# Kernel tuning notes

Hardware: AMD Instinct MI355X
Metric: run time of the kernel (lower is better)

## Reference

```python
import jax, jax.numpy as jnp
import numpy as np

N_NODES = 50000
N_EDGES = 800000
IN_FEATS = 128
OUT_FEATS = 64


def setup_inputs() -> dict:
    key = jax.random.key(0)
    k1, k2, k3, k4, k5, k6 = jax.random.split(key, 6)
    feat = jax.random.normal(k1, (N_NODES, IN_FEATS), dtype=jnp.float32)
    edge_src = jax.random.randint(k2, (N_EDGES,), 0, N_NODES, dtype=jnp.int64)
    edge_dst = jax.random.randint(k3, (N_EDGES,), 0, N_NODES, dtype=jnp.int64)
    eweight = jax.random.uniform(k4, (N_EDGES,), dtype=jnp.float32)
    W = jax.random.normal(k5, (OUT_FEATS, IN_FEATS), dtype=jnp.float32) * (1.0 / np.sqrt(IN_FEATS))
    b = jax.random.normal(k6, (OUT_FEATS,), dtype=jnp.float32) * 0.01
    return {"feat": feat, "edge_src": edge_src, "edge_dst": edge_dst,
            "eweight": eweight, "W": W, "b": b}


def reference(feat, edge_src, edge_dst, eweight, W, b):
    # Linear: [N, in] @ [in, out] + [out]
    h = jnp.einsum('ni,oi->no', feat, W) + b
    # u_mul_e: gather src features, scale by per-edge weight -> [E, out]
    m = h[edge_src] * eweight[:, None]
    # sum reduce over dst -> [N, out]
    out = jax.ops.segment_sum(m, edge_dst, num_segments=N_NODES)
    return out
```

## Files before the change

kernel.cpp:

```cpp
#include <hip/hip_runtime.h>

#define IN_FEATS 128
#define OUT_FEATS 64
#define TM 64
#define ALD 136
#define BW_LOG 6
#define BWIDTH 64
#define MAX_NB 1024
#define SE_PER_BLK 8192
#define MAX_BUCKET 3072

typedef short bf16x8 __attribute__((ext_vector_type(8)));
typedef float f32x4 __attribute__((ext_vector_type(4)));

__device__ inline unsigned short f2bf(float f) {
    unsigned u = __float_as_uint(f);
    u += 0x7FFFu + ((u >> 16) & 1u);
    return (unsigned short)(u >> 16);
}
__device__ inline float bf2f_lo(unsigned v) { return __uint_as_float(v << 16); }
__device__ inline float bf2f_hi(unsigned v) { return __uint_as_float(v & 0xFFFF0000u); }
__device__ inline ushort4 cvt4(float4 t) {
    ushort4 s; s.x = f2bf(t.x); s.y = f2bf(t.y); s.z = f2bf(t.z); s.w = f2bf(t.w);
    return s;
}

__global__ __launch_bounds__(256) void coarse_hist(
    const int* __restrict__ edst, int* __restrict__ ghist, int n_edges, int nb)
{
    __shared__ int hist[MAX_NB];
    const int tid = threadIdx.x;
    for (int i = tid; i < nb; i += 256) hist[i] = 0;
    __syncthreads();

    const int n4 = n_edges >> 2;
    const int4* ed4 = (const int4*)edst;
    for (int i = blockIdx.x * 256 + tid; i < n4; i += gridDim.x * 256) {
        int4 d = ed4[i];
        atomicAdd(&hist[d.x >> BW_LOG], 1);
        atomicAdd(&hist[d.y >> BW_LOG], 1);
        atomicAdd(&hist[d.z >> BW_LOG], 1);
        atomicAdd(&hist[d.w >> BW_LOG], 1);
    }
    if (blockIdx.x == 0 && tid < (n_edges & 3))
        atomicAdd(&hist[edst[n4 * 4 + tid] >> BW_LOG], 1);
    __syncthreads();
    for (int i = tid; i < nb; i += 256)
        if (hist[i]) atomicAdd(&ghist[i], hist[i]);
}

__global__ __launch_bounds__(256) void coarse_scan(
    const int* __restrict__ ghist, int* __restrict__ goff,
    int* __restrict__ gcur, int nb)
{
    __shared__ int wsum[4];
    __shared__ int wpre[4];
    const int tid  = threadIdx.x;
    const int lane = tid & 63;
    const int wv   = tid >> 6;
    int i0 = tid * 4;
    int v[4];
    int s = 0;
#pragma unroll
    for (int j = 0; j < 4; ++j) v[j] = (i0 + j < nb) ? ghist[i0 + j] : 0;
#pragma unroll
    for (int j = 0; j < 4; ++j) { int t = v[j]; v[j] = s; s += t; }
    int inc = s;
    for (int off = 1; off < 64; off <<= 1) {
        int t = __shfl_up(inc, off, 64);
        if (lane >= off) inc += t;
    }
    int wexcl = inc - s;
    if (lane == 63) wsum[wv] = inc;
    __syncthreads();
    if (tid == 0) {
        int a = 0;
        for (int k = 0; k < 4; ++k) { wpre[k] = a; a += wsum[k]; }
    }
    __syncthreads();
    int tbase = wpre[wv] + wexcl;
#pragma unroll
    for (int j = 0; j < 4; ++j) {
        int idx = i0 + j;
        if (idx < nb) { int e = tbase + v[j]; goff[idx] = e; gcur[idx] = e; }
    }
    if (tid == 0) goff[nb] = wpre[3] + wsum[3];
}

__global__ __launch_bounds__(256) void stage_linear(
    const float* __restrict__ feat, const float* __restrict__ W,
    const float* __restrict__ b, unsigned short* __restrict__ h,
    const int* __restrict__ esrc, const int* __restrict__ edst,
    const float* __restrict__ ew, int* __restrict__ gcur,
    int2* __restrict__ gstage, int n_nodes, int n_edges, int nb, int nstage)
{
    __shared__ union {
        struct { unsigned short As[TM * ALD]; unsigned short Ws[OUT_FEATS * ALD]; } lin;
        struct { int cntA[MAX_NB]; int cntB[MAX_NB]; int base[MAX_NB]; } st;
    } sm;
    const int tid = threadIdx.x;

    if ((int)blockIdx.x < nstage) {
        int* cntA = sm.st.cntA;
        int* cntB = sm.st.cntB;
        int* base = sm.st.base;
        const int e0 = blockIdx.x * SE_PER_BLK;
        const int e1 = min(e0 + SE_PER_BLK, n_edges);

        for (int i = tid; i < nb; i += 256) { cntA[i] = 0; cntB[i] = 0; }
        __syncthreads();
        for (int e = e0 + tid; e < e1; e += 256)
            atomicAdd(&cntA[edst[e] >> BW_LOG], 1);
        __syncthreads();
        for (int i = tid; i < nb; i += 256) {
            int c = cntA[i];
            base[i] = c ? atomicAdd(&gcur[i], c) : 0;
        }
        __syncthreads();
        for (int e = e0 + tid; e < e1; e += 256) {
            int d  = edst[e];
            int bb = d >> BW_LOG;
            int rk = atomicAdd(&cntB[bb], 1);
            gstage[base[bb] + rk] =
                make_int2(((d & (BWIDTH - 1)) << 16) | esrc[e],
                          __float_as_int(ew[e]));
        }
    } else {
        unsigned short* As = sm.lin.As;
        unsigned short* Ws = sm.lin.Ws;
        const int row0 = ((int)blockIdx.x - nstage) * TM;

        {
            const int c  = tid & 63;
            const int kb = (tid >> 6) * 32;
            const float4* wrow = (const float4*)(W + (size_t)c * IN_FEATS + kb);
#pragma unroll
            for (int i = 0; i < 8; ++i)
                *((ushort4*)&Ws[c * ALD + kb + i * 4]) = cvt4(wrow[i]);
        }
        {
#pragma unroll
            for (int i = 0; i < 8; ++i) {
                int flat = i * 256 + tid;
                int r  = flat >> 5;
                int kc = flat & 31;
                int gr = row0 + r;
                float4 t = (gr < n_nodes)
                    ? ((const float4*)(feat + (size_t)gr * IN_FEATS))[kc]
                    : make_float4(0.f, 0.f, 0.f, 0.f);
                *((ushort4*)&As[r * ALD + kc * 4]) = cvt4(t);
            }
        }
        __syncthreads();

        const int w    = tid >> 6;
        const int lane = tid & 63;
        const int m    = lane & 15;
        const int quad = lane >> 4;
        const int koff = quad * 8;

        f32x4 acc[4];
#pragma unroll
        for (int t = 0; t < 4; ++t) acc[t] = (f32x4){0.f, 0.f, 0.f, 0.f};

#pragma unroll
        for (int chunk = 0; chunk < 4; ++chunk) {
            const int kc = chunk * 32 + koff;
            bf16x8 a = *((const bf16x8*)&As[(w * 16 + m) * ALD + kc]);
#pragma unroll
            for (int t = 0; t < 4; ++t) {
                bf16x8 bfr = *((const bf16x8*)&Ws[(t * 16 + m) * ALD + kc]);
                acc[t] = __builtin_amdgcn_mfma_f32_16x16x32_bf16(a, bfr, acc[t], 0, 0, 0);
            }
        }

#pragma unroll
        for (int t = 0; t < 4; ++t) {
            const int col = t * 16 + m;
            const float bias = b[col];
#pragma unroll
            for (int i = 0; i < 4; ++i) {
                int r = row0 + w * 16 + quad * 4 + i;
                if (r < n_nodes)
                    h[(size_t)r * OUT_FEATS + col] = f2bf(acc[t][i] + bias);
            }
        }
    }
}

__global__ __launch_bounds__(256) void bin_sort(
    int2* __restrict__ gstage, const int* __restrict__ goff,
    int2* __restrict__ seg, int n_nodes, int nb)
{
    __shared__ int2 recs[MAX_BUCKET];
    __shared__ int cnt[BWIDTH];
    __shared__ int cur[BWIDTH];
    const int tid = threadIdx.x;
    const int b   = blockIdx.x;
    const int s0  = goff[b], s1 = goff[b + 1];
    const int m   = s1 - s0;

    if (tid < BWIDTH) cnt[tid] = 0;
    __syncthreads();

    for (int i = tid; i < m; i += 256) {
        int2 r = gstage[s0 + i];
        recs[i] = r;
        atomicAdd(&cnt[(r.x >> 16) & 63], 1);
    }
    __syncthreads();

    if (tid < 64) {
        int v = cnt[tid];
        int inc = v;
        for (int o = 1; o < 64; o <<= 1) {
            int t = __shfl_up(inc, o, 64);
            if (tid >= o) inc += t;
        }
        int excl = inc - v;
        cur[tid] = excl;
        int node = b * BWIDTH + tid;
        if (node < n_nodes) seg[node] = make_int2(s0 + excl, s0 + excl + v);
    }
    __syncthreads();

    for (int i = tid; i < m; i += 256) {
        int2 r = recs[i];
        int pos = atomicAdd(&cur[(r.x >> 16) & 63], 1);
        gstage[s0 + pos] = r;
    }
}

__global__ __launch_bounds__(256) void gather_kernel(
    const unsigned short* __restrict__ h, const int2* __restrict__ seg,
    const int2* __restrict__ perm2, float* __restrict__ out, int n_nodes)
{
    const int wid  = (blockIdx.x * blockDim.x + threadIdx.x) >> 6;
    const int lane = threadIdx.x & 63;
    const int g    = lane >> 5;
    const int f2   = lane & 31;
    const int node = wid * 2 + g;
    const unsigned* h32 = (const unsigned*)h;

    int2 se = (node < n_nodes) ? seg[node] : make_int2(0, 0);
    const int len = se.y - se.x;
    const int olen = __shfl_xor(len, 32, 64);
    const int omax = max(len, olen);

    float a0 = 0.f, a1 = 0.f;
    for (int u = 0; u < omax; u += 8) {
        int2 r[8]; unsigned hv[8];
#pragma unroll
        for (int k = 0; k < 8; ++k) {
            int uk  = u + k;
            int pos = (uk < len) ? (se.x + uk) : (len > 0 ? se.y - 1 : 0);
            r[k] = perm2[pos];
        }
#pragma unroll
        for (int k = 0; k < 8; ++k)
            hv[k] = h32[(size_t)(r[k].x & 0xFFFF) * 32 + f2];
#pragma unroll
        for (int k = 0; k < 8; ++k) {
            float w = (u + k < len) ? __int_as_float(r[k].y) : 0.f;
            a0 += w * bf2f_lo(hv[k]);
            a1 += w * bf2f_hi(hv[k]);
        }
    }
    if (node < n_nodes) {
        float2 o; o.x = a0; o.y = a1;
        *((float2*)&out[(size_t)node * OUT_FEATS + 2 * f2]) = o;
    }
}

__global__ __launch_bounds__(256) void scatter_kernel(
    const unsigned short* __restrict__ h, const int* __restrict__ esrc,
    const int* __restrict__ edst, const float* __restrict__ ew,
    float* __restrict__ out, int n_edges)
{
    const int lane = threadIdx.x & 63;
    const int wave = threadIdx.x >> 6;
    const int stride = gridDim.x * 4;
    for (int e = blockIdx.x * 4 + wave; e < n_edges; e += stride) {
        const int s = esrc[e];
        const int d = edst[e];
        const float w = ew[e];
        atomicAdd(out + (size_t)d * OUT_FEATS + lane,
                  bf2f_lo((unsigned)h[(size_t)s * OUT_FEATS + lane]) * w);
    }
}

extern "C" void kernel_launch(void* const* d_in, const int* in_sizes, int n_in,
                              void* d_out, int out_size, void* d_ws, size_t ws_size,
                              hipStream_t stream) {
    const float* feat = (const float*)d_in[0];
    const int*   esrc = (const int*)d_in[1];
    const int*   edst = (const int*)d_in[2];
    const float* ew   = (const float*)d_in[3];
    const float* W    = (const float*)d_in[4];
    const float* b    = (const float*)d_in[5];
    float* out = (float*)d_out;

    const int n_nodes = in_sizes[0] / IN_FEATS;
    const int n_edges = in_sizes[1];
    const int nb = (n_nodes + BWIDTH - 1) >> BW_LOG;
    const int nlin = (n_nodes + TM - 1) / TM;
    const int nstage = (n_edges + SE_PER_BLK - 1) / SE_PER_BLK;

    char* wsb = (char*)d_ws;
    unsigned short* h = (unsigned short*)wsb;
    size_t off_ghist = (((size_t)n_nodes * OUT_FEATS * sizeof(unsigned short)) + 15) & ~(size_t)15;
    size_t sz_ghist  = (((size_t)nb * sizeof(int)) + 15) & ~(size_t)15;
    size_t off_goff  = off_ghist + sz_ghist;
    size_t sz_goff   = (((size_t)(nb + 1) * sizeof(int)) + 15) & ~(size_t)15;
    size_t off_gcur  = off_goff + sz_goff;
    size_t sz_gcur   = (((size_t)nb * sizeof(int)) + 15) & ~(size_t)15;
    size_t off_seg   = off_gcur + sz_gcur;
    size_t sz_seg    = (((size_t)n_nodes * sizeof(int2)) + 15) & ~(size_t)15;
    size_t off_stage = off_seg + sz_seg;
    size_t needed    = off_stage + (size_t)n_edges * sizeof(int2);

    bool binnable = (nb <= MAX_NB) && (n_nodes < 65536) &&
                    ((size_t)n_edges / (size_t)nb * 2 + 256 <= MAX_BUCKET);

    if (ws_size >= needed && binnable) {
        int*  ghist  = (int*)(wsb + off_ghist);
        int*  goff   = (int*)(wsb + off_goff);
        int*  gcur   = (int*)(wsb + off_gcur);
        int2* seg    = (int2*)(wsb + off_seg);
        int2* gstage = (int2*)(wsb + off_stage);
        hipMemsetAsync(ghist, 0, (size_t)nb * sizeof(int), stream);
        coarse_hist<<<128, 256, 0, stream>>>(edst, ghist, n_edges, nb);
        coarse_scan<<<1, 256, 0, stream>>>(ghist, goff, gcur, nb);
        stage_linear<<<nstage + nlin, 256, 0, stream>>>(
            feat, W, b, h, esrc, edst, ew, gcur, gstage,
            n_nodes, n_edges, nb, nstage);
        bin_sort<<<nb, 256, 0, stream>>>(gstage, goff, seg, n_nodes, nb);
        const int gwaves = (n_nodes + 1) / 2;
        gather_kernel<<<(gwaves + 3) / 4, 256, 0, stream>>>(
            h, seg, gstage, out, n_nodes);
    } else {
        stage_linear<<<nlin, 256, 0, stream>>>(
            feat, W, b, h, esrc, edst, ew, nullptr, nullptr,
            n_nodes, n_edges, nb, 0);
        hipMemsetAsync(d_out, 0, (size_t)out_size * sizeof(float), stream);
        scatter_kernel<<<8192, 256, 0, stream>>>(h, esrc, edst, ew, out, n_edges);
    }
}
```

Before: 154.6 us.

## Register-cache staged edges and reuse first-pass atomic ranks for scatter

Each staging thread now loads 8 consecutive edges with vectorized int4/float4 loads, keeps them in registers, and records the rank returned by its single LDS atomicAdd pass. The second counting pass and its re-read of edge arrays are removed, and the scatter writes directly with the saved ranks. The per-block edge count drops to 2048, so there are four times as many staging blocks, each with fewer nb-sized init and global-atomic loops amortized over less work. Global atomics on gcur rise with the larger block count, and scatter order within a bucket changes.

```diff
diff --git a/kernel.cpp b/kernel.cpp
--- a/kernel.cpp
+++ b/kernel.cpp
@@ -7,7 +7,7 @@
 #define BW_LOG 6
 #define BWIDTH 64
 #define MAX_NB 1024
-#define SE_PER_BLK 8192
+#define SE_PER_BLK 2048
 #define MAX_BUCKET 3072
 
 typedef short bf16x8 __attribute__((ext_vector_type(8)));
@@ -96,34 +96,53 @@
 {
     __shared__ union {
         struct { unsigned short As[TM * ALD]; unsigned short Ws[OUT_FEATS * ALD]; } lin;
-        struct { int cntA[MAX_NB]; int cntB[MAX_NB]; int base[MAX_NB]; } st;
+        struct { int cnt[MAX_NB]; int base[MAX_NB]; } st;
     } sm;
     const int tid = threadIdx.x;
 
     if ((int)blockIdx.x < nstage) {
-        int* cntA = sm.st.cntA;
-        int* cntB = sm.st.cntB;
+        int* cnt  = sm.st.cnt;
         int* base = sm.st.base;
-        const int e0 = blockIdx.x * SE_PER_BLK;
-        const int e1 = min(e0 + SE_PER_BLK, n_edges);
-
-        for (int i = tid; i < nb; i += 256) { cntA[i] = 0; cntB[i] = 0; }
+        for (int i = tid; i < nb; i += 256) cnt[i] = 0;
         __syncthreads();
-        for (int e = e0 + tid; e < e1; e += 256)
-            atomicAdd(&cntA[edst[e] >> BW_LOG], 1);
+
+        const int e0 = blockIdx.x * SE_PER_BLK + tid * 8;
+        int dk[8]; int sk[8]; float wk[8]; int bk[8]; int rk[8];
+        if (e0 + 7 < n_edges) {
+            *((int4*)&dk[0]) = *((const int4*)&edst[e0]);
+            *((int4*)&dk[4]) = *((const int4*)&edst[e0 + 4]);
+            *((int4*)&sk[0]) = *((const int4*)&esrc[e0]);
+            *((int4*)&sk[4]) = *((const int4*)&esrc[e0 + 4]);
+            *((float4*)&wk[0]) = *((const float4*)&ew[e0]);
+            *((float4*)&wk[4]) = *((const float4*)&ew[e0 + 4]);
+#pragma unroll
+            for (int i = 0; i < 8; ++i) {
+                bk[i] = dk[i] >> BW_LOG;
+                rk[i] = atomicAdd(&cnt[bk[i]], 1);
+            }
+        } else {
+#pragma unroll
+            for (int i = 0; i < 8; ++i) {
+                int e = e0 + i;
+                if (e < n_edges) {
+                    dk[i] = edst[e]; sk[i] = esrc[e]; wk[i] = ew[e];
+                    bk[i] = dk[i] >> BW_LOG;
+                    rk[i] = atomicAdd(&cnt[bk[i]], 1);
+                } else bk[i] = -1;
+            }
+        }
         __syncthreads();
         for (int i = tid; i < nb; i += 256) {
-            int c = cntA[i];
+            int c = cnt[i];
             base[i] = c ? atomicAdd(&gcur[i], c) : 0;
         }
         __syncthreads();
-        for (int e = e0 + tid; e < e1; e += 256) {
-            int d  = edst[e];
-            int bb = d >> BW_LOG;
-            int rk = atomicAdd(&cntB[bb], 1);
-            gstage[base[bb] + rk] =
-                make_int2(((d & (BWIDTH - 1)) << 16) | esrc[e],
-                          __float_as_int(ew[e]));
+#pragma unroll
+        for (int i = 0; i < 8; ++i) {
+            if (bk[i] >= 0)
+                gstage[base[bk[i]] + rk[i]] =
+                    make_int2(((dk[i] & (BWIDTH - 1)) << 16) | sk[i],
+                              __float_as_int(wk[i]));
         }
     } else {
         unsigned short* As = sm.lin.As;
```

Result: faster. 146.1 us (-5.5%).
